# Kernel tuning notes

Measured on AMD Instinct MI355X. Metric: run time of the kernel, lower is better.

## Reference

```python
import jax, jax.numpy as jnp
import numpy as np

N_HEAD = 8
LN_EPS = 1e-5


def _ln(x, g, b):
    m = jnp.mean(x, axis=-1, keepdims=True)
    v = jnp.mean((x - m) ** 2, axis=-1, keepdims=True)
    return (x - m) * jax.lax.rsqrt(v + LN_EPS) * g + b


def setup_inputs() -> dict:
    B, S, IN, D, F, OUT, L = 4, 2048, 3, 512, 2048, 20, 6
    key = jax.random.key(0)
    ks = jax.random.split(key, 22)
    sc = 0.02
    return {
        'src': jax.random.normal(ks[0], (B, S, IN), jnp.float32),
        'W_in': jax.random.normal(ks[1], (IN, D), jnp.float32) * sc,
        'b_in': jnp.zeros((D,), jnp.float32),
        'Wq': jax.random.normal(ks[2], (L, D, D), jnp.float32) * sc,
        'bq': jnp.zeros((L, D), jnp.float32),
        'Wk': jax.random.normal(ks[3], (L, D, D), jnp.float32) * sc,
        'bk': jnp.zeros((L, D), jnp.float32),
        'Wv': jax.random.normal(ks[4], (L, D, D), jnp.float32) * sc,
        'bv': jnp.zeros((L, D), jnp.float32),
        'Wo': jax.random.normal(ks[5], (L, D, D), jnp.float32) * sc,
        'bo': jnp.zeros((L, D), jnp.float32),
        'ln1_g': jnp.ones((L, D), jnp.float32),
        'ln1_b': jnp.zeros((L, D), jnp.float32),
        'W1': jax.random.normal(ks[6], (L, D, F), jnp.float32) * sc,
        'b1': jnp.zeros((L, F), jnp.float32),
        'W2': jax.random.normal(ks[7], (L, F, D), jnp.float32) * sc,
        'b2': jnp.zeros((L, D), jnp.float32),
        'ln2_g': jnp.ones((L, D), jnp.float32),
        'ln2_b': jnp.zeros((L, D), jnp.float32),
        'W_out': jax.random.normal(ks[8], (D, OUT), jnp.float32) * sc,
        'b_out': jnp.zeros((OUT,), jnp.float32),
    }


def reference(src, W_in, b_in, Wq, bq, Wk, bk, Wv, bv, Wo, bo, ln1_g, ln1_b,
              W1, b1, W2, b2, ln2_g, ln2_b, W_out, b_out):
    x = src @ W_in + b_in            # [B, S, D]
    B, S, D = x.shape
    dh = D // N_HEAD
    scale = 1.0 / np.sqrt(dh).astype(np.float32)

    def layer(x, p):
        wq, biq, wk, bik, wv, biv, wo, bio, g1, be1, w1, bi1, w2, bi2, g2, be2 = p
        q = (x @ wq + biq).reshape(B, S, N_HEAD, dh)
        k = (x @ wk + bik).reshape(B, S, N_HEAD, dh)
        v = (x @ wv + biv).reshape(B, S, N_HEAD, dh)
        # flex_attention with score_mod=None == plain scaled dot-product attention
        scores = jnp.einsum('bqhd,bkhd->bhqk', q, k) * scale
        a = jax.nn.softmax(scores, axis=-1)
        o = jnp.einsum('bhqk,bkhd->bqhd', a, v).reshape(B, S, D)
        attn = o @ wo + bio
        h = _ln(x + attn, g1, be1)                       # post-norm (norm_first=False)
        ff = jax.nn.relu(h @ w1 + bi1) @ w2 + bi2
        h = _ln(h + ff, g2, be2)
        return h, None

    x, _ = jax.lax.scan(layer, x, (Wq, bq, Wk, bk, Wv, bv, Wo, bo,
                                   ln1_g, ln1_b, W1, b1, W2, b2, ln2_g, ln2_b))
    return x @ W_out + b_out         # [B, S, OUT]
```

## Files before the change

kernel.cpp:

```cpp
#include <hip/hip_runtime.h>

typedef unsigned short u16;
typedef unsigned int u32;
typedef __bf16 bf16x8 __attribute__((ext_vector_type(8)));
typedef float f32x4 __attribute__((ext_vector_type(4)));
typedef float f32x16 __attribute__((ext_vector_type(16)));

__device__ __forceinline__ u16 f2bf(float f) {
    union { float f; u32 u; } v; v.f = f;
    u32 r = v.u + 0x7FFFu + ((v.u >> 16) & 1u);
    return (u16)(r >> 16);
}

__device__ __forceinline__ u16 bfu(float x) {
    __bf16 b = (__bf16)x;
    union { __bf16 b; u16 u; } c; c.b = b; return c.u;
}

__device__ __forceinline__ float max3f(float a, float b, float c) {
    return fmaxf(fmaxf(a, b), c);
}

__device__ __forceinline__ void gload16(const u16* g, u16* l) {
    __builtin_amdgcn_global_load_lds((const __attribute__((address_space(1))) void*)g,
                                     (__attribute__((address_space(3))) void*)l, 16, 0, 0);
}

__global__ void wtrans(const float* __restrict__ W, u16* __restrict__ Wt,
                       int K, int N, int rowOff, int dstLd, long long dstStride)
{
    __shared__ float tile[32][33];
    const int l = blockIdx.z;
    const float* Wl = W + (size_t)l * K * N;
    u16* Wtl = Wt + (size_t)l * dstStride;
    const int tx = threadIdx.x, ty = threadIdx.y;
    const int x = blockIdx.x * 32 + tx;
    const int y0 = blockIdx.y * 32;
#pragma unroll
    for (int j = 0; j < 32; j += 8) tile[ty + j][tx] = Wl[(size_t)(y0 + ty + j) * N + x];
    __syncthreads();
    const int n0 = blockIdx.x * 32;
    const int k = y0 + tx;
#pragma unroll
    for (int j = 0; j < 32; j += 8)
        Wtl[(size_t)(rowOff + n0 + ty + j) * dstLd + k] = f2bf(tile[tx][ty + j]);
}

__global__ __launch_bounds__(256) void input_proj(const float* __restrict__ src,
    const float* __restrict__ Wi, const float* __restrict__ bi,
    float* __restrict__ xf, u16* __restrict__ xb)
{
    int idx = blockIdx.x * 256 + threadIdx.x;
    int m = idx >> 9, n = idx & 511;
    float v = bi[n] + src[m * 3] * Wi[n] + src[m * 3 + 1] * Wi[512 + n] + src[m * 3 + 2] * Wi[1024 + n];
    xf[idx] = v;
    xb[idx] = f2bf(v);
}

template<int EPI>
__global__ __launch_bounds__(256) void gemm_bt(
    const u16* __restrict__ A, const u16* __restrict__ Bt,
    const float* __restrict__ bias,
    float* __restrict__ Cf, u16* __restrict__ Cb,
    u16* __restrict__ Qo, u16* __restrict__ Ko, u16* __restrict__ Vo,
    const float* __restrict__ bq, const float* __restrict__ bk, const float* __restrict__ bv,
    int M, int N, int K)
{
    __shared__ u16 As[128 * 32];
    __shared__ u16 Bs[128 * 32];
    const int tid = threadIdx.x;
    const int lane = tid & 63, wid = tid >> 6;
    const int bn = blockIdx.x, bm = blockIdx.y;
    const int row0 = bm * 128, col0 = bn * 128;
    const int srow = lane >> 2, skc = lane & 3;
    const int c0 = wid * 2, c1 = wid * 2 + 1;
    const u16* gA0 = A + (size_t)(row0 + c0 * 16 + srow) * K + skc * 8;
    const u16* gA1 = A + (size_t)(row0 + c1 * 16 + srow) * K + skc * 8;
    const u16* gB0 = Bt + (size_t)(col0 + c0 * 16 + srow) * K + skc * 8;
    const u16* gB1 = Bt + (size_t)(col0 + c1 * 16 + srow) * K + skc * 8;
    u16* lA0 = &As[c0 * 512]; u16* lA1 = &As[c1 * 512];
    u16* lB0 = &Bs[c0 * 512]; u16* lB1 = &Bs[c1 * 512];
    const int wr = (wid >> 1) * 64, wc = (wid & 1) * 64;
    const int cc = lane & 15, qg = lane >> 4;
    const int arow0 = (wr + cc) * 32 + qg * 8;
    const int brow0 = (wc + cc) * 32 + qg * 8;
    f32x4 acc[4][4] = {};
    for (int k0 = 0; k0 < K; k0 += 32) {
        __syncthreads();
        gload16(gA0 + k0, lA0);
        gload16(gA1 + k0, lA1);
        gload16(gB0 + k0, lB0);
        gload16(gB1 + k0, lB1);
        __syncthreads();
        bf16x8 af[4], bfr[4];
#pragma unroll
        for (int i = 0; i < 4; i++) af[i] = *(const bf16x8*)&As[arow0 + i * 512];
#pragma unroll
        for (int i = 0; i < 4; i++) bfr[i] = *(const bf16x8*)&Bs[brow0 + i * 512];
#pragma unroll
        for (int mi = 0; mi < 4; mi++)
#pragma unroll
            for (int ni = 0; ni < 4; ni++)
                acc[mi][ni] = __builtin_amdgcn_mfma_f32_16x16x32_bf16(af[mi], bfr[ni], acc[mi][ni], 0, 0, 0);
    }
    const int q4 = qg * 4;
    if (EPI == 2) {
#pragma unroll
        for (int mi = 0; mi < 4; mi++) {
            int grow = row0 + wr + mi * 16 + q4;
            int btok = grow >> 11, srem = grow & 2047;
#pragma unroll
            for (int ni = 0; ni < 4; ni++) {
                int gcol = col0 + wc + ni * 16 + cc;
                int sec = gcol >> 9, f = gcol & 511;
                int hh = f >> 6, dd = f & 63;
                if (sec == 0) {
                    float bb = bq[f];
                    size_t base = (((size_t)btok * 8 + hh) * 2048 + srem) * 64 + dd;
#pragma unroll
                    for (int i = 0; i < 4; i++) Qo[base + (size_t)i * 64] = f2bf((acc[mi][ni][i] + bb) * 0.18033688f);
                } else if (sec == 1) {
                    float bb = bk[f];
                    size_t base = (((size_t)btok * 8 + hh) * 2048 + srem) * 64 + dd;
#pragma unroll
                    for (int i = 0; i < 4; i++) Ko[base + (size_t)i * 64] = f2bf(acc[mi][ni][i] + bb);
                } else {
                    float bb = bv[f];
                    size_t base = (((size_t)btok * 8 + hh) * 64 + dd) * 2048 + srem;
#pragma unroll
                    for (int i = 0; i < 4; i++) Vo[base + i] = f2bf(acc[mi][ni][i] + bb);
                }
            }
        }
    } else {
#pragma unroll
        for (int mi = 0; mi < 4; mi++) {
            int grow = row0 + wr + mi * 16 + q4;
#pragma unroll
            for (int ni = 0; ni < 4; ni++) {
                int gcol = col0 + wc + ni * 16 + cc;
                float bb = bias[gcol];
#pragma unroll
                for (int i = 0; i < 4; i++) {
                    float v = acc[mi][ni][i] + bb;
                    if (EPI == 0) Cf[(size_t)(grow + i) * N + gcol] = v;
                    else          Cb[(size_t)(grow + i) * N + gcol] = f2bf(v > 0.f ? v : 0.f);
                }
            }
        }
    }
}

__global__ __launch_bounds__(256) void gemm_bt_n64(
    const u16* __restrict__ A, const u16* __restrict__ Bt,
    const float* __restrict__ bias, float* __restrict__ Cf,
    int M, int N, int K)
{
    __shared__ u16 As[128 * 32];
    __shared__ u16 Bs[64 * 32];
    const int tid = threadIdx.x;
    const int lane = tid & 63, wid = tid >> 6;
    const int bn = blockIdx.x, bm = blockIdx.y;
    const int row0 = bm * 128, col0 = bn * 64;
    const int srow = lane >> 2, skc = lane & 3;
    const int c0 = wid * 2, c1 = wid * 2 + 1;
    const u16* gA0 = A + (size_t)(row0 + c0 * 16 + srow) * K + skc * 8;
    const u16* gA1 = A + (size_t)(row0 + c1 * 16 + srow) * K + skc * 8;
    const u16* gB  = Bt + (size_t)(col0 + (tid >> 2)) * K + (tid & 3) * 8;
    u16* lA0 = &As[c0 * 512]; u16* lA1 = &As[c1 * 512];
    u16* lB  = &Bs[tid * 8];
    const int wr = (wid >> 1) * 64, wc = (wid & 1) * 32;
    const int cc = lane & 15, qg = lane >> 4;
    const int arow0 = (wr + cc) * 32 + qg * 8;
    const int brow0 = (wc + cc) * 32 + qg * 8;
    f32x4 acc[4][2] = {};
    for (int k0 = 0; k0 < K; k0 += 32) {
        __syncthreads();
        gload16(gA0 + k0, lA0);
        gload16(gA1 + k0, lA1);
        gload16(gB + k0, lB);
        __syncthreads();
        bf16x8 af[4], bfr[2];
#pragma unroll
        for (int i = 0; i < 4; i++) af[i] = *(const bf16x8*)&As[arow0 + i * 512];
#pragma unroll
        for (int i = 0; i < 2; i++) bfr[i] = *(const bf16x8*)&Bs[brow0 + i * 512];
#pragma unroll
        for (int mi = 0; mi < 4; mi++)
#pragma unroll
            for (int ni = 0; ni < 2; ni++)
                acc[mi][ni] = __builtin_amdgcn_mfma_f32_16x16x32_bf16(af[mi], bfr[ni], acc[mi][ni], 0, 0, 0);
    }
    const int q4 = qg * 4;
#pragma unroll
    for (int mi = 0; mi < 4; mi++) {
        int grow = row0 + wr + mi * 16 + q4;
#pragma unroll
        for (int ni = 0; ni < 2; ni++) {
            int gcol = col0 + wc + ni * 16 + cc;
            float bb = bias[gcol];
#pragma unroll
            for (int i = 0; i < 4; i++)
                Cf[(size_t)(grow + i) * N + gcol] = acc[mi][ni][i] + bb;
        }
    }
}

__global__ __launch_bounds__(256, 2) void flash_attn(
    const u16* __restrict__ Qb, const u16* __restrict__ Kb, const u16* __restrict__ Vt,
    u16* __restrict__ Ob)
{
    __shared__ u16 Ks[2][4096];
    __shared__ u16 Vs[2][4096];
    const int tid = threadIdx.x, lane = tid & 63, w = tid >> 6;
    const int l31 = lane & 31, h = lane >> 5;
    const int bh = blockIdx.x, qt = blockIdx.y;
    const u16* Kg = Kb + (size_t)bh * (2048 * 64);
    const u16* Vg = Vt + (size_t)bh * (64 * 2048);

    bf16x8 qf[4];
    {
        const u16* Qrow = Qb + ((size_t)bh * 2048 + (size_t)qt * 128 + w * 32 + l31) * 64;
#pragma unroll
        for (int f = 0; f < 4; f++) qf[f] = *(const bf16x8*)(Qrow + f * 16 + h * 8);
    }
    f32x16 os0{}, os1{};
    float mrun = -1e30f, lrun = 0.f;

    const int r8 = lane >> 3;
    const int cswz = ((lane & 7) ^ r8) * 8;
#pragma unroll
    for (int cc = 0; cc < 2; cc++) {
        int c = w * 2 + cc;
        gload16(Kg + (size_t)(c * 8 + r8) * 64 + cswz, &Ks[0][c * 512]);
        gload16(Vg + (size_t)(c * 8 + r8) * 2048 + cswz, &Vs[0][c * 512]);
    }
    const int swz = (l31 & 7) << 3;

    for (int kt = 0; kt < 32; kt++) {
        const int cur = kt & 1;
        asm volatile("s_waitcnt vmcnt(0)" ::: "memory");
        __syncthreads();
        if (kt < 31) {
#pragma unroll
            for (int cc = 0; cc < 2; cc++) {
                int c = w * 2 + cc;
                gload16(Kg + (size_t)(kt + 1) * 4096 + (size_t)(c * 8 + r8) * 64 + cswz, &Ks[cur ^ 1][c * 512]);
                gload16(Vg + (size_t)(c * 8 + r8) * 2048 + (size_t)(kt + 1) * 64 + cswz, &Vs[cur ^ 1][c * 512]);
            }
        }
        f32x16 p0{}, p1{};
        {
            const u16* kb = &Ks[cur][0];
#pragma unroll
            for (int f = 0; f < 4; f++) {
                int colu = (f * 16 + h * 8) ^ swz;
                bf16x8 ka0 = *(const bf16x8*)(kb + l31 * 64 + colu);
                bf16x8 ka1 = *(const bf16x8*)(kb + (32 + l31) * 64 + colu);
                p0 = __builtin_amdgcn_mfma_f32_32x32x16_bf16(ka0, qf[f], p0, 0, 0, 0);
                p1 = __builtin_amdgcn_mfma_f32_32x32x16_bf16(ka1, qf[f], p1, 0, 0, 0);
            }
        }
        float a0 = max3f(p0[0], p0[1], p0[2]);
        float a1 = max3f(p0[3], p0[4], p0[5]);
        float a2 = max3f(p0[6], p0[7], p0[8]);
        float a3 = max3f(p0[9], p0[10], p0[11]);
        float a4 = max3f(p0[12], p0[13], p0[14]);
        float a5 = max3f(p0[15], p1[0], p1[1]);
        float a6 = max3f(p1[2], p1[3], p1[4]);
        float a7 = max3f(p1[5], p1[6], p1[7]);
        float a8 = max3f(p1[8], p1[9], p1[10]);
        float a9 = max3f(p1[11], p1[12], p1[13]);
        float b0 = max3f(a0, a1, a2);
        float b1 = max3f(a3, a4, a5);
        float b2 = max3f(a6, a7, a8);
        float b3 = max3f(a9, p1[14], p1[15]);
        float mx = fmaxf(max3f(b0, b1, b2), b3);
        mx = fmaxf(mx, __shfl_xor(mx, 32));
        if (!__all(mx <= mrun + 8.f)) {
            float mn = fmaxf(mrun, mx);
            float al = __builtin_amdgcn_exp2f(mrun - mn);
            os0 *= al; os1 *= al; lrun *= al; mrun = mn;
        }
        float sum = 0.f;
#pragma unroll
        for (int r = 0; r < 16; r++) { float e = __builtin_amdgcn_exp2f(p0[r] - mrun); p0[r] = e; sum += e; }
#pragma unroll
        for (int r = 0; r < 16; r++) { float e = __builtin_amdgcn_exp2f(p1[r] - mrun); p1[r] = e; sum += e; }
        sum += __shfl_xor(sum, 32);
        lrun += sum;
        const u16* vb = &Vs[cur][0];
#pragma unroll
        for (int t = 0; t < 2; t++) {
            u32 pk[8], sw[8];
#pragma unroll
            for (int j = 0; j < 8; j++) {
                float a = t ? p1[2 * j] : p0[2 * j];
                float b = t ? p1[2 * j + 1] : p0[2 * j + 1];
                pk[j] = (u32)bfu(a) | ((u32)bfu(b) << 16);
                sw[j] = __shfl_xor(pk[j], 32);
            }
            union { u32 u[4]; bf16x8 v; } fA, fB;
            fA.u[0] = h ? sw[2] : pk[0];
            fA.u[1] = h ? sw[3] : pk[1];
            fA.u[2] = h ? pk[2] : sw[0];
            fA.u[3] = h ? pk[3] : sw[1];
            fB.u[0] = h ? sw[6] : pk[4];
            fB.u[1] = h ? sw[7] : pk[5];
            fB.u[2] = h ? pk[6] : sw[4];
            fB.u[3] = h ? pk[7] : sw[5];
#pragma unroll
            for (int f = 0; f < 2; f++) {
                bf16x8 pa = f ? fB.v : fA.v;
                int colu = (t * 32 + f * 16 + h * 8) ^ swz;
                bf16x8 v0 = *(const bf16x8*)(vb + l31 * 64 + colu);
                bf16x8 v1 = *(const bf16x8*)(vb + (32 + l31) * 64 + colu);
                os0 = __builtin_amdgcn_mfma_f32_32x32x16_bf16(pa, v0, os0, 0, 0, 0);
                os1 = __builtin_amdgcn_mfma_f32_32x32x16_bf16(pa, v1, os1, 0, 0, 0);
            }
        }
    }
    float rl = 1.f / lrun;
    const int hatt = bh & 7, b_ = bh >> 3;
#pragma unroll
    for (int r = 0; r < 16; r++) {
        int qrow = (r & 3) + 8 * (r >> 2) + 4 * h;
        float rlq = __shfl(rl, qrow);
        int tok = qt * 128 + w * 32 + qrow;
        u16* po = Ob + ((size_t)b_ * 2048 + tok) * 512 + hatt * 64;
        po[l31] = bfu(os0[r] * rlq);
        po[32 + l31] = bfu(os1[r] * rlq);
    }
}

__global__ __launch_bounds__(256) void ln_res(
    const float* __restrict__ X, const float* __restrict__ Y,
    const float* __restrict__ g, const float* __restrict__ bta,
    float* __restrict__ Of, u16* __restrict__ Ob)
{
    const int lane = threadIdx.x & 63;
    const int row = blockIdx.x * 4 + (threadIdx.x >> 6);
    const size_t base = (size_t)row * 512 + lane * 8;
    float4 x0 = *(const float4*)(X + base);
    float4 x1 = *(const float4*)(X + base + 4);
    float4 y0 = *(const float4*)(Y + base);
    float4 y1 = *(const float4*)(Y + base + 4);
    float t[8] = {x0.x + y0.x, x0.y + y0.y, x0.z + y0.z, x0.w + y0.w,
                  x1.x + y1.x, x1.y + y1.y, x1.z + y1.z, x1.w + y1.w};
    float s = 0.f, s2 = 0.f;
#pragma unroll
    for (int j = 0; j < 8; j++) { s += t[j]; s2 += t[j] * t[j]; }
#pragma unroll
    for (int off = 1; off < 64; off <<= 1) { s += __shfl_xor(s, off); s2 += __shfl_xor(s2, off); }
    float mean = s * (1.f / 512.f);
    float var = s2 * (1.f / 512.f) - mean * mean;
    float rs = rsqrtf(var + 1e-5f);
    float4 g0 = *(const float4*)(g + lane * 8);
    float4 g1 = *(const float4*)(g + lane * 8 + 4);
    float4 b0 = *(const float4*)(bta + lane * 8);
    float4 b1 = *(const float4*)(bta + lane * 8 + 4);
    float gg[8] = {g0.x, g0.y, g0.z, g0.w, g1.x, g1.y, g1.z, g1.w};
    float bb[8] = {b0.x, b0.y, b0.z, b0.w, b1.x, b1.y, b1.z, b1.w};
    float o[8];
#pragma unroll
    for (int j = 0; j < 8; j++) o[j] = (t[j] - mean) * rs * gg[j] + bb[j];
    *(float4*)(Of + base) = make_float4(o[0], o[1], o[2], o[3]);
    *(float4*)(Of + base + 4) = make_float4(o[4], o[5], o[6], o[7]);
    u32 p0 = (u32)f2bf(o[0]) | ((u32)f2bf(o[1]) << 16);
    u32 p1 = (u32)f2bf(o[2]) | ((u32)f2bf(o[3]) << 16);
    u32 p2 = (u32)f2bf(o[4]) | ((u32)f2bf(o[5]) << 16);
    u32 p3 = (u32)f2bf(o[6]) | ((u32)f2bf(o[7]) << 16);
    *(uint4*)(Ob + base) = make_uint4(p0, p1, p2, p3);
}

__global__ __launch_bounds__(320) void out_proj(const float* __restrict__ x,
    const float* __restrict__ W, const float* __restrict__ b, float* __restrict__ out)
{
    int t = blockIdx.x * 320 + threadIdx.x;
    int m = t / 20, o = t - m * 20;
    const float* xr = x + (size_t)m * 512;
    float acc = b[o];
#pragma unroll 8
    for (int k = 0; k < 512; k++) acc = fmaf(xr[k], W[k * 20 + o], acc);
    out[(size_t)m * 20 + o] = acc;
}

extern "C" void kernel_launch(void* const* d_in, const int* in_sizes, int n_in,
                              void* d_out, int out_size, void* d_ws, size_t ws_size,
                              hipStream_t stream)
{
    const float* src  = (const float*)d_in[0];
    const float* W_in = (const float*)d_in[1];
    const float* b_in = (const float*)d_in[2];
    const float* Wq   = (const float*)d_in[3];
    const float* bq   = (const float*)d_in[4];
    const float* Wk   = (const float*)d_in[5];
    const float* bk   = (const float*)d_in[6];
    const float* Wv   = (const float*)d_in[7];
    const float* bv   = (const float*)d_in[8];
    const float* Wo   = (const float*)d_in[9];
    const float* bo   = (const float*)d_in[10];
    const float* ln1g = (const float*)d_in[11];
    const float* ln1b = (const float*)d_in[12];
    const float* W1   = (const float*)d_in[13];
    const float* b1   = (const float*)d_in[14];
    const float* W2   = (const float*)d_in[15];
    const float* b2   = (const float*)d_in[16];
    const float* ln2g = (const float*)d_in[17];
    const float* ln2b = (const float*)d_in[18];
    const float* Wout = (const float*)d_in[19];
    const float* bout = (const float*)d_in[20];

    char* ws = (char*)d_ws;
    size_t off = 0;
    auto take = [&](size_t bytes) -> void* {
        off = (off + 255) & ~(size_t)255;
        void* p = ws + off;
        off += bytes;
        return p;
    };
    const size_t TOK = 8192, D = 512;
    u16*   qkvt = (u16*)take(6ull * 1536 * 512 * 2);
    u16*   wot  = (u16*)take(6ull * 512 * 512 * 2);
    u16*   w1t  = (u16*)take(6ull * 2048 * 512 * 2);
    u16*   w2t  = (u16*)take(6ull * 512 * 2048 * 2);
    float* xf   = (float*)take(TOK * D * 4);
    u16*   xb   = (u16*)take(TOK * D * 2);
    u16*   sh4  = (u16*)take(4ull * TOK * D * 2);
    float* scr  = (float*)take(TOK * D * 4);
    float* h1f  = (float*)take(TOK * D * 4);
    u16*   h1b  = (u16*)take(TOK * D * 2);
    if (off > ws_size) return;

    u16* qb  = sh4;
    u16* kb_ = sh4 + TOK * D;
    u16* vtb = sh4 + 2 * TOK * D;
    u16* ob  = sh4 + 3 * TOK * D;
    u16* ffb = sh4;

    dim3 tb(32, 8);
    wtrans<<<dim3(16, 16, 6), tb, 0, stream>>>(Wq, qkvt, 512, 512, 0,    512, 1536ll * 512);
    wtrans<<<dim3(16, 16, 6), tb, 0, stream>>>(Wk, qkvt, 512, 512, 512,  512, 1536ll * 512);
    wtrans<<<dim3(16, 16, 6), tb, 0, stream>>>(Wv, qkvt, 512, 512, 1024, 512, 1536ll * 512);
    wtrans<<<dim3(16, 16, 6), tb, 0, stream>>>(Wo, wot,  512, 512, 0,    512, 512ll * 512);
    wtrans<<<dim3(64, 16, 6), tb, 0, stream>>>(W1, w1t,  512, 2048, 0,   512, 2048ll * 512);
    wtrans<<<dim3(16, 64, 6), tb, 0, stream>>>(W2, w2t,  2048, 512, 0,  2048, 512ll * 2048);

    input_proj<<<16384, 256, 0, stream>>>(src, W_in, b_in, xf, xb);

    for (int l = 0; l < 6; l++) {
        const u16* qkvt_l = qkvt + (size_t)l * 1536 * 512;
        const u16* wot_l  = wot  + (size_t)l * 512 * 512;
        const u16* w1t_l  = w1t  + (size_t)l * 2048 * 512;
        const u16* w2t_l  = w2t  + (size_t)l * 512 * 2048;

        gemm_bt<2><<<dim3(12, 64), 256, 0, stream>>>(xb, qkvt_l, nullptr,
            nullptr, nullptr, qb, kb_, vtb,
            bq + l * 512, bk + l * 512, bv + l * 512, 8192, 1536, 512);

        flash_attn<<<dim3(32, 16), 256, 0, stream>>>(qb, kb_, vtb, ob);

        gemm_bt_n64<<<dim3(8, 64), 256, 0, stream>>>(ob, wot_l, bo + l * 512,
            scr, 8192, 512, 512);

        ln_res<<<2048, 256, 0, stream>>>(xf, scr, ln1g + l * 512, ln1b + l * 512, h1f, h1b);

        gemm_bt<1><<<dim3(16, 64), 256, 0, stream>>>(h1b, w1t_l, b1 + l * 2048,
            nullptr, ffb, nullptr, nullptr, nullptr, nullptr, nullptr, nullptr,
            8192, 2048, 512);

        gemm_bt_n64<<<dim3(8, 64), 256, 0, stream>>>(ffb, w2t_l, b2 + l * 512,
            scr, 8192, 512, 2048);

        ln_res<<<2048, 256, 0, stream>>>(h1f, scr, ln2g + l * 512, ln2b + l * 512, xf, xb);
    }

    out_proj<<<512, 320, 0, stream>>>(xf, Wout, bout, (float*)d_out);
}
```

Measured before the change: 1.222 ms.

## Process two KV tiles per flash-attention iteration and widen n64 GEMM K-step

The flash attention loop now handles two 64-key tiles per iteration using four LDS buffers, so barriers and the online-softmax max/rescale run half as often. It also adds s_setprio around the MFMA blocks and splits the exp sum across eight accumulators. The n64 GEMM now loads K=64 per step with XOR-swizzled LDS to halve syncs and avoid bank conflicts. The cost is twice the LDS per attention block (64KB) and more registers, which may lower occupancy.

```diff
diff --git a/kernel.cpp b/kernel.cpp
--- a/kernel.cpp
+++ b/kernel.cpp
@@ -19,6 +19,17 @@
 
 __device__ __forceinline__ float max3f(float a, float b, float c) {
     return fmaxf(fmaxf(a, b), c);
+}
+
+__device__ __forceinline__ float vmax16(const f32x16& p) {
+    float a0 = max3f(p[0], p[1], p[2]);
+    float a1 = max3f(p[3], p[4], p[5]);
+    float a2 = max3f(p[6], p[7], p[8]);
+    float a3 = max3f(p[9], p[10], p[11]);
+    float a4 = max3f(p[12], p[13], p[14]);
+    float b0 = max3f(a0, a1, a2);
+    float b1 = max3f(a3, a4, p[15]);
+    return fmaxf(b0, b1);
 }
 
 __device__ __forceinline__ void gload16(const u16* g, u16* l) {
@@ -156,40 +167,55 @@
     const float* __restrict__ bias, float* __restrict__ Cf,
     int M, int N, int K)
 {
-    __shared__ u16 As[128 * 32];
-    __shared__ u16 Bs[64 * 32];
+    __shared__ u16 As[128 * 64];
+    __shared__ u16 Bs[64 * 64];
     const int tid = threadIdx.x;
     const int lane = tid & 63, wid = tid >> 6;
-    const int bn = blockIdx.x, bm = blockIdx.y;
-    const int row0 = bm * 128, col0 = bn * 64;
-    const int srow = lane >> 2, skc = lane & 3;
-    const int c0 = wid * 2, c1 = wid * 2 + 1;
-    const u16* gA0 = A + (size_t)(row0 + c0 * 16 + srow) * K + skc * 8;
-    const u16* gA1 = A + (size_t)(row0 + c1 * 16 + srow) * K + skc * 8;
-    const u16* gB  = Bt + (size_t)(col0 + (tid >> 2)) * K + (tid & 3) * 8;
-    u16* lA0 = &As[c0 * 512]; u16* lA1 = &As[c1 * 512];
-    u16* lB  = &Bs[tid * 8];
+    const int row0 = blockIdx.y * 128, col0 = blockIdx.x * 64;
     const int wr = (wid >> 1) * 64, wc = (wid & 1) * 32;
     const int cc = lane & 15, qg = lane >> 4;
-    const int arow0 = (wr + cc) * 32 + qg * 8;
-    const int brow0 = (wc + cc) * 32 + qg * 8;
     f32x4 acc[4][2] = {};
-    for (int k0 = 0; k0 < K; k0 += 32) {
+    for (int k0 = 0; k0 < K; k0 += 64) {
         __syncthreads();
-        gload16(gA0 + k0, lA0);
-        gload16(gA1 + k0, lA1);
-        gload16(gB + k0, lB);
+#pragma unroll
+        for (int j = 0; j < 4; j++) {
+            int s = j * 256 + tid;
+            int r = s >> 3, g = s & 7;
+            gload16(A + (size_t)(row0 + r) * K + k0 + (g ^ (r & 7)) * 8, &As[s * 8]);
+        }
+#pragma unroll
+        for (int j = 0; j < 2; j++) {
+            int s = j * 256 + tid;
+            int r = s >> 3, g = s & 7;
+            gload16(Bt + (size_t)(col0 + r) * K + k0 + (g ^ (r & 7)) * 8, &Bs[s * 8]);
+        }
         __syncthreads();
-        bf16x8 af[4], bfr[2];
-#pragma unroll
-        for (int i = 0; i < 4; i++) af[i] = *(const bf16x8*)&As[arow0 + i * 512];
-#pragma unroll
-        for (int i = 0; i < 2; i++) bfr[i] = *(const bf16x8*)&Bs[brow0 + i * 512];
+        bf16x8 af[4][2], bfr[2][2];
+#pragma unroll
+        for (int i = 0; i < 4; i++) {
+            int r = wr + i * 16 + cc;
+#pragma unroll
+            for (int kk = 0; kk < 2; kk++) {
+                int g = kk * 4 + qg;
+                af[i][kk] = *(const bf16x8*)&As[r * 64 + (g ^ (r & 7)) * 8];
+            }
+        }
+#pragma unroll
+        for (int i = 0; i < 2; i++) {
+            int r = wc + i * 16 + cc;
+#pragma unroll
+            for (int kk = 0; kk < 2; kk++) {
+                int g = kk * 4 + qg;
+                bfr[i][kk] = *(const bf16x8*)&Bs[r * 64 + (g ^ (r & 7)) * 8];
+            }
+        }
 #pragma unroll
         for (int mi = 0; mi < 4; mi++)
 #pragma unroll
-            for (int ni = 0; ni < 2; ni++)
-                acc[mi][ni] = __builtin_amdgcn_mfma_f32_16x16x32_bf16(af[mi], bfr[ni], acc[mi][ni], 0, 0, 0);
+            for (int ni = 0; ni < 2; ni++) {
+                acc[mi][ni] = __builtin_amdgcn_mfma_f32_16x16x32_bf16(af[mi][0], bfr[ni][0], acc[mi][ni], 0, 0, 0);
+                acc[mi][ni] = __builtin_amdgcn_mfma_f32_16x16x32_bf16(af[mi][1], bfr[ni][1], acc[mi][ni], 0, 0, 0);
+            }
     }
     const int q4 = qg * 4;
 #pragma unroll
@@ -210,8 +236,8 @@
     const u16* __restrict__ Qb, const u16* __restrict__ Kb, const u16* __restrict__ Vt,
     u16* __restrict__ Ob)
 {
-    __shared__ u16 Ks[2][4096];
-    __shared__ u16 Vs[2][4096];
+    __shared__ u16 Ks[4][4096];
+    __shared__ u16 Vs[4][4096];
     const int tid = threadIdx.x, lane = tid & 63, w = tid >> 6;
     const int l31 = lane & 31, h = lane >> 5;
     const int bh = blockIdx.x, qt = blockIdx.y;
@@ -230,93 +256,101 @@
     const int r8 = lane >> 3;
     const int cswz = ((lane & 7) ^ r8) * 8;
 #pragma unroll
-    for (int cc = 0; cc < 2; cc++) {
-        int c = w * 2 + cc;
-        gload16(Kg + (size_t)(c * 8 + r8) * 64 + cswz, &Ks[0][c * 512]);
-        gload16(Vg + (size_t)(c * 8 + r8) * 2048 + cswz, &Vs[0][c * 512]);
-    }
+    for (int u = 0; u < 2; u++)
+#pragma unroll
+        for (int cc = 0; cc < 2; cc++) {
+            int c = w * 2 + cc;
+            gload16(Kg + (size_t)u * 4096 + (size_t)(c * 8 + r8) * 64 + cswz, &Ks[u][c * 512]);
+            gload16(Vg + (size_t)(c * 8 + r8) * 2048 + (size_t)u * 64 + cswz, &Vs[u][c * 512]);
+        }
     const int swz = (l31 & 7) << 3;
 
-    for (int kt = 0; kt < 32; kt++) {
-        const int cur = kt & 1;
+    for (int it = 0; it < 16; it++) {
+        const int bp = (it & 1) << 1;
         asm volatile("s_waitcnt vmcnt(0)" ::: "memory");
         __syncthreads();
-        if (kt < 31) {
-#pragma unroll
-            for (int cc = 0; cc < 2; cc++) {
-                int c = w * 2 + cc;
-                gload16(Kg + (size_t)(kt + 1) * 4096 + (size_t)(c * 8 + r8) * 64 + cswz, &Ks[cur ^ 1][c * 512]);
-                gload16(Vg + (size_t)(c * 8 + r8) * 2048 + (size_t)(kt + 1) * 64 + cswz, &Vs[cur ^ 1][c * 512]);
-            }
-        }
-        f32x16 p0{}, p1{};
+        if (it < 15) {
+#pragma unroll
+            for (int u = 0; u < 2; u++) {
+                int kt = 2 * it + 2 + u, bq_ = (bp ^ 2) + u;
+#pragma unroll
+                for (int cc = 0; cc < 2; cc++) {
+                    int c = w * 2 + cc;
+                    gload16(Kg + (size_t)kt * 4096 + (size_t)(c * 8 + r8) * 64 + cswz, &Ks[bq_][c * 512]);
+                    gload16(Vg + (size_t)(c * 8 + r8) * 2048 + (size_t)kt * 64 + cswz, &Vs[bq_][c * 512]);
+                }
+            }
+        }
+        f32x16 p0{}, p1{}, p2{}, p3{};
         {
-            const u16* kb = &Ks[cur][0];
+            const u16* ka = &Ks[bp][0];
+            const u16* kb = &Ks[bp + 1][0];
+            __builtin_amdgcn_s_setprio(1);
 #pragma unroll
             for (int f = 0; f < 4; f++) {
                 int colu = (f * 16 + h * 8) ^ swz;
-                bf16x8 ka0 = *(const bf16x8*)(kb + l31 * 64 + colu);
-                bf16x8 ka1 = *(const bf16x8*)(kb + (32 + l31) * 64 + colu);
-                p0 = __builtin_amdgcn_mfma_f32_32x32x16_bf16(ka0, qf[f], p0, 0, 0, 0);
-                p1 = __builtin_amdgcn_mfma_f32_32x32x16_bf16(ka1, qf[f], p1, 0, 0, 0);
-            }
-        }
-        float a0 = max3f(p0[0], p0[1], p0[2]);
-        float a1 = max3f(p0[3], p0[4], p0[5]);
-        float a2 = max3f(p0[6], p0[7], p0[8]);
-        float a3 = max3f(p0[9], p0[10], p0[11]);
-        float a4 = max3f(p0[12], p0[13], p0[14]);
-        float a5 = max3f(p0[15], p1[0], p1[1]);
-        float a6 = max3f(p1[2], p1[3], p1[4]);
-        float a7 = max3f(p1[5], p1[6], p1[7]);
-        float a8 = max3f(p1[8], p1[9], p1[10]);
-        float a9 = max3f(p1[11], p1[12], p1[13]);
-        float b0 = max3f(a0, a1, a2);
-        float b1 = max3f(a3, a4, a5);
-        float b2 = max3f(a6, a7, a8);
-        float b3 = max3f(a9, p1[14], p1[15]);
-        float mx = fmaxf(max3f(b0, b1, b2), b3);
+                bf16x8 a0 = *(const bf16x8*)(ka + l31 * 64 + colu);
+                bf16x8 a1 = *(const bf16x8*)(ka + (32 + l31) * 64 + colu);
+                bf16x8 b0 = *(const bf16x8*)(kb + l31 * 64 + colu);
+                bf16x8 b1 = *(const bf16x8*)(kb + (32 + l31) * 64 + colu);
+                p0 = __builtin_amdgcn_mfma_f32_32x32x16_bf16(a0, qf[f], p0, 0, 0, 0);
+                p1 = __builtin_amdgcn_mfma_f32_32x32x16_bf16(a1, qf[f], p1, 0, 0, 0);
+                p2 = __builtin_amdgcn_mfma_f32_32x32x16_bf16(b0, qf[f], p2, 0, 0, 0);
+                p3 = __builtin_amdgcn_mfma_f32_32x32x16_bf16(b1, qf[f], p3, 0, 0, 0);
+            }
+            __builtin_amdgcn_s_setprio(0);
+        }
+        float mx = fmaxf(fmaxf(vmax16(p0), vmax16(p1)), fmaxf(vmax16(p2), vmax16(p3)));
         mx = fmaxf(mx, __shfl_xor(mx, 32));
         if (!__all(mx <= mrun + 8.f)) {
             float mn = fmaxf(mrun, mx);
             float al = __builtin_amdgcn_exp2f(mrun - mn);
             os0 *= al; os1 *= al; lrun *= al; mrun = mn;
         }
-        float sum = 0.f;
-#pragma unroll
-        for (int r = 0; r < 16; r++) { float e = __builtin_amdgcn_exp2f(p0[r] - mrun); p0[r] = e; sum += e; }
-#pragma unroll
-        for (int r = 0; r < 16; r++) { float e = __builtin_amdgcn_exp2f(p1[r] - mrun); p1[r] = e; sum += e; }
+        float ss[8] = {};
+#pragma unroll
+        for (int r = 0; r < 16; r++) { float e = __builtin_amdgcn_exp2f(p0[r] - mrun); p0[r] = e; ss[r & 7] += e; }
+#pragma unroll
+        for (int r = 0; r < 16; r++) { float e = __builtin_amdgcn_exp2f(p1[r] - mrun); p1[r] = e; ss[r & 7] += e; }
+#pragma unroll
+        for (int r = 0; r < 16; r++) { float e = __builtin_amdgcn_exp2f(p2[r] - mrun); p2[r] = e; ss[r & 7] += e; }
+#pragma unroll
+        for (int r = 0; r < 16; r++) { float e = __builtin_amdgcn_exp2f(p3[r] - mrun); p3[r] = e; ss[r & 7] += e; }
+        float sum = ((ss[0] + ss[1]) + (ss[2] + ss[3])) + ((ss[4] + ss[5]) + (ss[6] + ss[7]));
         sum += __shfl_xor(sum, 32);
         lrun += sum;
-        const u16* vb = &Vs[cur][0];
-#pragma unroll
-        for (int t = 0; t < 2; t++) {
-            u32 pk[8], sw[8];
-#pragma unroll
-            for (int j = 0; j < 8; j++) {
-                float a = t ? p1[2 * j] : p0[2 * j];
-                float b = t ? p1[2 * j + 1] : p0[2 * j + 1];
-                pk[j] = (u32)bfu(a) | ((u32)bfu(b) << 16);
-                sw[j] = __shfl_xor(pk[j], 32);
-            }
-            union { u32 u[4]; bf16x8 v; } fA, fB;
-            fA.u[0] = h ? sw[2] : pk[0];
-            fA.u[1] = h ? sw[3] : pk[1];
-            fA.u[2] = h ? pk[2] : sw[0];
-            fA.u[3] = h ? pk[3] : sw[1];
-            fB.u[0] = h ? sw[6] : pk[4];
-            fB.u[1] = h ? sw[7] : pk[5];
-            fB.u[2] = h ? pk[6] : sw[4];
-            fB.u[3] = h ? pk[7] : sw[5];
-#pragma unroll
-            for (int f = 0; f < 2; f++) {
-                bf16x8 pa = f ? fB.v : fA.v;
-                int colu = (t * 32 + f * 16 + h * 8) ^ swz;
-                bf16x8 v0 = *(const bf16x8*)(vb + l31 * 64 + colu);
-                bf16x8 v1 = *(const bf16x8*)(vb + (32 + l31) * 64 + colu);
-                os0 = __builtin_amdgcn_mfma_f32_32x32x16_bf16(pa, v0, os0, 0, 0, 0);
-                os1 = __builtin_amdgcn_mfma_f32_32x32x16_bf16(pa, v1, os1, 0, 0, 0);
+#pragma unroll
+        for (int u = 0; u < 2; u++) {
+            const u16* vb = &Vs[bp + u][0];
+#pragma unroll
+            for (int t = 0; t < 2; t++) {
+                const f32x16& qq = u ? (t ? p3 : p2) : (t ? p1 : p0);
+                u32 pk[8], sw[8];
+#pragma unroll
+                for (int j = 0; j < 8; j++) {
+                    pk[j] = (u32)bfu(qq[2 * j]) | ((u32)bfu(qq[2 * j + 1]) << 16);
+                    sw[j] = __shfl_xor(pk[j], 32);
+                }
+                union { u32 u[4]; bf16x8 v; } fA, fB;
+                fA.u[0] = h ? sw[2] : pk[0];
+                fA.u[1] = h ? sw[3] : pk[1];
+                fA.u[2] = h ? pk[2] : sw[0];
+                fA.u[3] = h ? pk[3] : sw[1];
+                fB.u[0] = h ? sw[6] : pk[4];
+                fB.u[1] = h ? sw[7] : pk[5];
+                fB.u[2] = h ? pk[6] : sw[4];
+                fB.u[3] = h ? pk[7] : sw[5];
+                __builtin_amdgcn_s_setprio(1);
+#pragma unroll
+                for (int f = 0; f < 2; f++) {
+                    bf16x8 pa = f ? fB.v : fA.v;
+                    int colu = (t * 32 + f * 16 + h * 8) ^ swz;
+                    bf16x8 v0 = *(const bf16x8*)(vb + l31 * 64 + colu);
+                    bf16x8 v1 = *(const bf16x8*)(vb + (32 + l31) * 64 + colu);
+                    os0 = __builtin_amdgcn_mfma_f32_32x32x16_bf16(pa, v0, os0, 0, 0, 0);
+                    os1 = __builtin_amdgcn_mfma_f32_32x32x16_bf16(pa, v1, os1, 0, 0, 0);
+                }
+                __builtin_amdgcn_s_setprio(0);
             }
         }
     }
```

New measurement: 1.181 ms. -3.3%, faster.
